# Kernel tuning notes

Measured on AMD Instinct MI355X. Metric: run time of the kernel, lower is better.

Reference implementation:

```python
import jax, jax.numpy as jnp
import numpy as np


def conv1x1(x, w, b):
    # x: [B, Cin, D, H, W], w: [Cout, Cin], b: [Cout]
    return jnp.einsum('bcdhw,oc->bodhw', x, w) + b[None, :, None, None, None]


def setup_inputs() -> dict:
    key = jax.random.key(0)
    ks = jax.random.split(key, 9)
    B, C, D, H, W = 2, 64, 16, 16, 16
    Cc = 64          # context_dim
    C8 = C // 8      # inner attention dim
    s = 0.05
    return {
        'x': jax.random.normal(ks[0], (B, C, D, H, W), jnp.float32),
        'context': jax.random.normal(ks[1], (B, Cc, D, H, W), jnp.float32),
        'Wq': jax.random.normal(ks[2], (C8, C), jnp.float32) * s,
        'bq': jax.random.normal(ks[3], (C8,), jnp.float32) * s,
        'Wk': jax.random.normal(ks[4], (C8, Cc), jnp.float32) * s,
        'bk': jax.random.normal(ks[5], (C8,), jnp.float32) * s,
        'Wv': jax.random.normal(ks[6], (C, Cc), jnp.float32) * s,
        'bv': jax.random.normal(ks[7], (C,), jnp.float32) * s,
        'gamma': jax.random.normal(ks[8], (1,), jnp.float32) * s,
    }


def reference(x, context, Wq, bq, Wk, bk, Wv, bv, gamma):
    B, C, D, H, W = x.shape
    N = D * H * W
    q = conv1x1(x, Wq, bq).reshape(B, -1, N)        # [B, C/8, N]
    k = conv1x1(context, Wk, bk).reshape(B, -1, N)  # [B, C/8, N]
    v = conv1x1(context, Wv, bv).reshape(B, C, N)   # [B, C, N]
    # energy[b, n, m] = q[:, :, n] . k[:, :, m]  (no scaling, as in source)
    energy = jnp.einsum('bcn,bcm->bnm', q, k)       # [B, N, N]
    attn = jax.nn.softmax(energy, axis=-1)
    # out = v @ attn^T : out[b, c, n] = sum_m v[b, c, m] * attn[b, n, m]
    out = jnp.einsum('bcm,bnm->bcn', v, attn).reshape(B, C, D, H, W)
    return gamma[0] * out + x
```

## Files before the change

### kernel.cpp

```cpp
#include <hip/hip_runtime.h>

#define NTOK 4096

typedef __attribute__((ext_vector_type(8))) short short8;
typedef __attribute__((ext_vector_type(4))) float f32x4;
typedef __attribute__((ext_vector_type(4))) unsigned int uint4v;

__device__ __forceinline__ unsigned short f2bf(float f) {
    unsigned u = __float_as_uint(f);
    u += 0x7fffu + ((u >> 16) & 1u);
    return (unsigned short)(u >> 16);
}

__device__ __forceinline__ unsigned int pk2(float lo, float hi) {
    return __builtin_amdgcn_perm(__float_as_uint(hi), __float_as_uint(lo), 0x07060302u);
}

__global__ __launch_bounds__(256) void proj(
    const float* __restrict__ x, const float* __restrict__ ctx,
    const float* __restrict__ Wq, const float* __restrict__ bq,
    const float* __restrict__ Wk, const float* __restrict__ bk,
    const float* __restrict__ Wv, const float* __restrict__ bv,
    unsigned short* __restrict__ qbf32, unsigned short* __restrict__ kbf32,
    unsigned short* __restrict__ vtp)
{
    __shared__ float sW[16 * 64];
    __shared__ float sB[16];
    int tid  = threadIdx.x;
    int ogrp = blockIdx.z;
    int b    = blockIdx.y;
    int n0   = blockIdx.x * 64;

    if (ogrp == 0) {
        for (int i = tid; i < 1024; i += 256)
            sW[i] = (i < 512) ? Wq[i] : Wk[i - 512];
        if (tid < 16) sB[tid] = (tid < 8) ? bq[tid] : bk[tid - 8];
    } else {
        for (int i = tid; i < 1024; i += 256)
            sW[i] = Wv[(ogrp - 1) * 1024 + i];
        if (tid < 16) sB[tid] = bv[(ogrp - 1) * 16 + tid];
    }
    __syncthreads();

    int nn   = tid & 63;
    int osub = tid >> 6;
    const float* inp = (ogrp == 0 && osub < 2) ? x : ctx;
    const float* ip  = inp + (size_t)b * 64 * NTOK + n0 + nn;

    float a0 = sB[osub * 4 + 0], a1 = sB[osub * 4 + 1];
    float a2 = sB[osub * 4 + 2], a3 = sB[osub * 4 + 3];
#pragma unroll 16
    for (int c = 0; c < 64; ++c) {
        float val = ip[(size_t)c * NTOK];
        a0 += sW[(osub * 4 + 0) * 64 + c] * val;
        a1 += sW[(osub * 4 + 1) * 64 + c] * val;
        a2 += sW[(osub * 4 + 2) * 64 + c] * val;
        a3 += sW[(osub * 4 + 3) * 64 + c] * val;
    }
    float av[4] = {a0, a1, a2, a3};

    if (ogrp == 0) {
        bool isq = osub < 2;
        float sc = isq ? 1.4426950408889634f : 1.0f;
        unsigned short* dst = isq ? qbf32 : kbf32;
        int half = osub & 1;
        size_t base = ((size_t)b * NTOK + n0 + nn) * 32;
        ushort4 pk = {f2bf(av[0] * sc), f2bf(av[1] * sc), f2bf(av[2] * sc), f2bf(av[3] * sc)};
        *(ushort4*)&dst[base + half * 4] = pk;
        ushort4 z = {0, 0, 0, 0};
        if (half == 0) {
            *(ushort4*)&dst[base + 8]  = z;
            *(ushort4*)&dst[base + 12] = z;
            *(ushort4*)&dst[base + 16] = z;
        } else {
            *(ushort4*)&dst[base + 20] = z;
            *(ushort4*)&dst[base + 24] = z;
            *(ushort4*)&dst[base + 28] = z;
        }
    } else {
        int cbase = (ogrp - 1) * 16 + osub * 4;
        int m  = n0 + nn;
        int g  = m & ~31;
        int mm = m & 31;
        int p  = ((mm >> 2) & 3) * 8 + (mm >> 4) * 4 + (mm & 3);
#pragma unroll
        for (int j = 0; j < 4; ++j)
            vtp[((size_t)b * 64 + cbase + j) * NTOK + g + p] = f2bf(av[j]);
    }
}

__global__ __launch_bounds__(512, 4) void attn3(
    const unsigned short* __restrict__ qbf32, const unsigned short* __restrict__ kbf32,
    const unsigned short* __restrict__ vtp, const float* __restrict__ x,
    const float* __restrict__ gamma, float* __restrict__ out)
{
    __shared__ float sO[8][64][17];
    __shared__ float sL[8][16];

    int tid  = threadIdx.x;
    int w    = tid >> 6, lane = tid & 63;
    int n    = lane & 15, quad = lane >> 4;
    int b    = blockIdx.y;
    int n0   = blockIdx.x * 16;

    const f32x4 z4 = {0.f, 0.f, 0.f, 0.f};
    short8 bq = *(const short8*)&qbf32[((size_t)b * NTOK + n0 + n) * 32 + quad * 8];

    const unsigned short* kb = kbf32 + (size_t)b * NTOK * 32;
    const unsigned short* vb = vtp   + (size_t)b * 64 * NTOK;
    int mbase = w * 512;

#define KLD(h, t) (*(const short8*)&kb[((size_t)(mbase + (h) * 64 + (t) * 16 + n)) * 32 + quad * 8])
#define VLD(h, s, ct) (*(const short8*)&vb[(size_t)((ct) * 16 + n) * NTOK + mbase + (h) * 64 + (s) * 32 + quad * 8])

    f32x4 acc0 = z4, acc1 = z4, acc2 = z4, acc3 = z4;
    float lsum = 0.f;

    short8 kf0 = KLD(0, 0), kf1 = KLD(0, 1), kf2 = KLD(0, 2), kf3 = KLD(0, 3);
    short8 af0 = VLD(0, 0, 0), af1 = VLD(0, 0, 1), af2 = VLD(0, 0, 2), af3 = VLD(0, 0, 3);
    short8 af4 = VLD(0, 1, 0), af5 = VLD(0, 1, 1), af6 = VLD(0, 1, 2), af7 = VLD(0, 1, 3);

    for (int h = 0; h < 8; ++h) {
        f32x4 sa0 = __builtin_amdgcn_mfma_f32_16x16x32_bf16(kf0, bq, z4, 0, 0, 0);
        f32x4 sa1 = __builtin_amdgcn_mfma_f32_16x16x32_bf16(kf1, bq, z4, 0, 0, 0);
        f32x4 sa2 = __builtin_amdgcn_mfma_f32_16x16x32_bf16(kf2, bq, z4, 0, 0, 0);
        f32x4 sa3 = __builtin_amdgcn_mfma_f32_16x16x32_bf16(kf3, bq, z4, 0, 0, 0);
        if (h < 7) {
            kf0 = KLD(h + 1, 0); kf1 = KLD(h + 1, 1);
            kf2 = KLD(h + 1, 2); kf3 = KLD(h + 1, 3);
        }

        float e00 = exp2f(sa0[0]), e01 = exp2f(sa0[1]), e02 = exp2f(sa0[2]), e03 = exp2f(sa0[3]);
        float e10 = exp2f(sa1[0]), e11 = exp2f(sa1[1]), e12 = exp2f(sa1[2]), e13 = exp2f(sa1[3]);
        float e20 = exp2f(sa2[0]), e21 = exp2f(sa2[1]), e22 = exp2f(sa2[2]), e23 = exp2f(sa2[3]);
        float e30 = exp2f(sa3[0]), e31 = exp2f(sa3[1]), e32 = exp2f(sa3[2]), e33 = exp2f(sa3[3]);
        lsum += ((e00 + e01) + (e02 + e03)) + ((e10 + e11) + (e12 + e13))
              + ((e20 + e21) + (e22 + e23)) + ((e30 + e31) + (e32 + e33));

        uint4v t0, t1;
        t0[0] = pk2(e00, e01); t0[1] = pk2(e02, e03);
        t0[2] = pk2(e10, e11); t0[3] = pk2(e12, e13);
        t1[0] = pk2(e20, e21); t1[1] = pk2(e22, e23);
        t1[2] = pk2(e30, e31); t1[3] = pk2(e32, e33);
        short8 pf0 = __builtin_bit_cast(short8, t0);
        short8 pf1 = __builtin_bit_cast(short8, t1);

        acc0 = __builtin_amdgcn_mfma_f32_16x16x32_bf16(af0, pf0, acc0, 0, 0, 0);
        acc1 = __builtin_amdgcn_mfma_f32_16x16x32_bf16(af1, pf0, acc1, 0, 0, 0);
        acc2 = __builtin_amdgcn_mfma_f32_16x16x32_bf16(af2, pf0, acc2, 0, 0, 0);
        acc3 = __builtin_amdgcn_mfma_f32_16x16x32_bf16(af3, pf0, acc3, 0, 0, 0);
        acc0 = __builtin_amdgcn_mfma_f32_16x16x32_bf16(af4, pf1, acc0, 0, 0, 0);
        acc1 = __builtin_amdgcn_mfma_f32_16x16x32_bf16(af5, pf1, acc1, 0, 0, 0);
        acc2 = __builtin_amdgcn_mfma_f32_16x16x32_bf16(af6, pf1, acc2, 0, 0, 0);
        acc3 = __builtin_amdgcn_mfma_f32_16x16x32_bf16(af7, pf1, acc3, 0, 0, 0);

        if (h < 7) {
            af0 = VLD(h + 1, 0, 0); af1 = VLD(h + 1, 0, 1);
            af2 = VLD(h + 1, 0, 2); af3 = VLD(h + 1, 0, 3);
            af4 = VLD(h + 1, 1, 0); af5 = VLD(h + 1, 1, 1);
            af6 = VLD(h + 1, 1, 2); af7 = VLD(h + 1, 1, 3);
        }
    }
#undef KLD
#undef VLD

    lsum += __shfl_xor(lsum, 16);
    lsum += __shfl_xor(lsum, 32);
    if (lane < 16) sL[w][n] = lsum;
    f32x4 acc[4] = {acc0, acc1, acc2, acc3};
#pragma unroll
    for (int ct = 0; ct < 4; ++ct)
#pragma unroll
        for (int r = 0; r < 4; ++r)
            sO[w][ct * 16 + quad * 4 + r][n] = acc[ct][r];
    __syncthreads();

    int c  = tid >> 3;
    int ng = (tid & 7) * 2;
    float g = gamma[0];
    float L0 = 0.f, L1 = 0.f, v0 = 0.f, v1 = 0.f;
#pragma unroll
    for (int w2 = 0; w2 < 8; ++w2) {
        L0 += sL[w2][ng];     L1 += sL[w2][ng + 1];
        v0 += sO[w2][c][ng];  v1 += sO[w2][c][ng + 1];
    }
    size_t ob = ((size_t)b * 64 + c) * NTOK + n0 + ng;
    float2 xv = *(const float2*)&x[ob];
    float2 ov = {g * (v0 / L0) + xv.x, g * (v1 / L1) + xv.y};
    *(float2*)&out[ob] = ov;
}

extern "C" void kernel_launch(void* const* d_in, const int* in_sizes, int n_in,
                              void* d_out, int out_size, void* d_ws, size_t ws_size,
                              hipStream_t stream) {
    const float* x     = (const float*)d_in[0];
    const float* ctx   = (const float*)d_in[1];
    const float* Wq    = (const float*)d_in[2];
    const float* bq    = (const float*)d_in[3];
    const float* Wk    = (const float*)d_in[4];
    const float* bk    = (const float*)d_in[5];
    const float* Wv    = (const float*)d_in[6];
    const float* bv    = (const float*)d_in[7];
    const float* gamma = (const float*)d_in[8];
    float* out = (float*)d_out;

    unsigned short* qbf32 = (unsigned short*)d_ws;
    unsigned short* kbf32 = qbf32 + 2 * NTOK * 32;
    unsigned short* vtp   = kbf32 + 2 * NTOK * 32;

    proj<<<dim3(64, 2, 5), 256, 0, stream>>>(x, ctx, Wq, bq, Wk, bk, Wv, bv, qbf32, kbf32, vtp);
    attn3<<<dim3(NTOK / 16, 2), 512, 0, stream>>>(qbf32, kbf32, vtp, x, gamma, out);
}
```

Before: 114.6 us.

## Compact Q/K to 8 bf16, split keys across 16 waves, use native exp2

Q and K are now stored as 8 bf16 values per token instead of a zero-padded 32. Only lanes with quad==0 load them, and the other lanes feed zeros into the MFMA, which cuts the memory traffic for padding and the zero-fill stores in the projection kernel. The attention kernel now runs 1024 threads with 16 waves, each covering 256 keys instead of 512, which doubles parallel work per block at the cost of more shared memory and a 16-way reduction. exp2f is replaced by the hardware exp2 builtin to avoid range-handling code.

```diff
diff --git a/kernel.cpp b/kernel.cpp
--- a/kernel.cpp
+++ b/kernel.cpp
@@ -21,7 +21,7 @@
     const float* __restrict__ Wq, const float* __restrict__ bq,
     const float* __restrict__ Wk, const float* __restrict__ bk,
     const float* __restrict__ Wv, const float* __restrict__ bv,
-    unsigned short* __restrict__ qbf32, unsigned short* __restrict__ kbf32,
+    unsigned short* __restrict__ qbf, unsigned short* __restrict__ kbf,
     unsigned short* __restrict__ vtp)
 {
     __shared__ float sW[16 * 64];
@@ -62,21 +62,10 @@
     if (ogrp == 0) {
         bool isq = osub < 2;
         float sc = isq ? 1.4426950408889634f : 1.0f;
-        unsigned short* dst = isq ? qbf32 : kbf32;
+        unsigned short* dst = isq ? qbf : kbf;
         int half = osub & 1;
-        size_t base = ((size_t)b * NTOK + n0 + nn) * 32;
         ushort4 pk = {f2bf(av[0] * sc), f2bf(av[1] * sc), f2bf(av[2] * sc), f2bf(av[3] * sc)};
-        *(ushort4*)&dst[base + half * 4] = pk;
-        ushort4 z = {0, 0, 0, 0};
-        if (half == 0) {
-            *(ushort4*)&dst[base + 8]  = z;
-            *(ushort4*)&dst[base + 12] = z;
-            *(ushort4*)&dst[base + 16] = z;
-        } else {
-            *(ushort4*)&dst[base + 20] = z;
-            *(ushort4*)&dst[base + 24] = z;
-            *(ushort4*)&dst[base + 28] = z;
-        }
+        *(ushort4*)&dst[((size_t)b * NTOK + n0 + nn) * 8 + half * 4] = pk;
     } else {
         int cbase = (ogrp - 1) * 16 + osub * 4;
         int m  = n0 + nn;
@@ -89,13 +78,13 @@
     }
 }
 
-__global__ __launch_bounds__(512, 4) void attn3(
-    const unsigned short* __restrict__ qbf32, const unsigned short* __restrict__ kbf32,
+__global__ __launch_bounds__(1024, 8) void attn4(
+    const unsigned short* __restrict__ qbf, const unsigned short* __restrict__ kbf,
     const unsigned short* __restrict__ vtp, const float* __restrict__ x,
     const float* __restrict__ gamma, float* __restrict__ out)
 {
-    __shared__ float sO[8][64][17];
-    __shared__ float sL[8][16];
+    __shared__ float sO[16][64][17];
+    __shared__ float sL[16][16];
 
     int tid  = threadIdx.x;
     int w    = tid >> 6, lane = tid & 63;
@@ -104,13 +93,17 @@
     int n0   = blockIdx.x * 16;
 
     const f32x4 z4 = {0.f, 0.f, 0.f, 0.f};
-    short8 bq = *(const short8*)&qbf32[((size_t)b * NTOK + n0 + n) * 32 + quad * 8];
-
-    const unsigned short* kb = kbf32 + (size_t)b * NTOK * 32;
-    const unsigned short* vb = vtp   + (size_t)b * 64 * NTOK;
-    int mbase = w * 512;
-
-#define KLD(h, t) (*(const short8*)&kb[((size_t)(mbase + (h) * 64 + (t) * 16 + n)) * 32 + quad * 8])
+    const short8 z8 = {0, 0, 0, 0, 0, 0, 0, 0};
+
+    short8 bq = z8;
+    if (quad == 0)
+        bq = *(const short8*)&qbf[((size_t)b * NTOK + n0 + n) * 8];
+
+    const unsigned short* kb = kbf + (size_t)b * NTOK * 8;
+    const unsigned short* vb = vtp + (size_t)b * 64 * NTOK;
+    int mbase = w * 256;
+
+#define KLD(h, t) (quad == 0 ? *(const short8*)&kb[(size_t)(mbase + (h) * 64 + (t) * 16 + n) * 8] : z8)
 #define VLD(h, s, ct) (*(const short8*)&vb[(size_t)((ct) * 16 + n) * NTOK + mbase + (h) * 64 + (s) * 32 + quad * 8])
 
     f32x4 acc0 = z4, acc1 = z4, acc2 = z4, acc3 = z4;
@@ -120,20 +113,24 @@
     short8 af0 = VLD(0, 0, 0), af1 = VLD(0, 0, 1), af2 = VLD(0, 0, 2), af3 = VLD(0, 0, 3);
     short8 af4 = VLD(0, 1, 0), af5 = VLD(0, 1, 1), af6 = VLD(0, 1, 2), af7 = VLD(0, 1, 3);
 
-    for (int h = 0; h < 8; ++h) {
+    for (int h = 0; h < 4; ++h) {
         f32x4 sa0 = __builtin_amdgcn_mfma_f32_16x16x32_bf16(kf0, bq, z4, 0, 0, 0);
         f32x4 sa1 = __builtin_amdgcn_mfma_f32_16x16x32_bf16(kf1, bq, z4, 0, 0, 0);
         f32x4 sa2 = __builtin_amdgcn_mfma_f32_16x16x32_bf16(kf2, bq, z4, 0, 0, 0);
         f32x4 sa3 = __builtin_amdgcn_mfma_f32_16x16x32_bf16(kf3, bq, z4, 0, 0, 0);
-        if (h < 7) {
+        if (h < 3) {
             kf0 = KLD(h + 1, 0); kf1 = KLD(h + 1, 1);
             kf2 = KLD(h + 1, 2); kf3 = KLD(h + 1, 3);
         }
 
-        float e00 = exp2f(sa0[0]), e01 = exp2f(sa0[1]), e02 = exp2f(sa0[2]), e03 = exp2f(sa0[3]);
-        float e10 = exp2f(sa1[0]), e11 = exp2f(sa1[1]), e12 = exp2f(sa1[2]), e13 = exp2f(sa1[3]);
-        float e20 = exp2f(sa2[0]), e21 = exp2f(sa2[1]), e22 = exp2f(sa2[2]), e23 = exp2f(sa2[3]);
-        float e30 = exp2f(sa3[0]), e31 = exp2f(sa3[1]), e32 = exp2f(sa3[2]), e33 = exp2f(sa3[3]);
+        float e00 = __builtin_amdgcn_exp2f(sa0[0]), e01 = __builtin_amdgcn_exp2f(sa0[1]);
+        float e02 = __builtin_amdgcn_exp2f(sa0[2]), e03 = __builtin_amdgcn_exp2f(sa0[3]);
+        float e10 = __builtin_amdgcn_exp2f(sa1[0]), e11 = __builtin_amdgcn_exp2f(sa1[1]);
+        float e12 = __builtin_amdgcn_exp2f(sa1[2]), e13 = __builtin_amdgcn_exp2f(sa1[3]);
+        float e20 = __builtin_amdgcn_exp2f(sa2[0]), e21 = __builtin_amdgcn_exp2f(sa2[1]);
+        float e22 = __builtin_amdgcn_exp2f(sa2[2]), e23 = __builtin_amdgcn_exp2f(sa2[3]);
+        float e30 = __builtin_amdgcn_exp2f(sa3[0]), e31 = __builtin_amdgcn_exp2f(sa3[1]);
+        float e32 = __builtin_amdgcn_exp2f(sa3[2]), e33 = __builtin_amdgcn_exp2f(sa3[3]);
         lsum += ((e00 + e01) + (e02 + e03)) + ((e10 + e11) + (e12 + e13))
               + ((e20 + e21) + (e22 + e23)) + ((e30 + e31) + (e32 + e33));
 
@@ -154,7 +151,7 @@
         acc2 = __builtin_amdgcn_mfma_f32_16x16x32_bf16(af6, pf1, acc2, 0, 0, 0);
         acc3 = __builtin_amdgcn_mfma_f32_16x16x32_bf16(af7, pf1, acc3, 0, 0, 0);
 
-        if (h < 7) {
+        if (h < 3) {
             af0 = VLD(h + 1, 0, 0); af1 = VLD(h + 1, 0, 1);
             af2 = VLD(h + 1, 0, 2); af3 = VLD(h + 1, 0, 3);
             af4 = VLD(h + 1, 1, 0); af5 = VLD(h + 1, 1, 1);
@@ -175,19 +172,17 @@
             sO[w][ct * 16 + quad * 4 + r][n] = acc[ct][r];
     __syncthreads();
 
-    int c  = tid >> 3;
-    int ng = (tid & 7) * 2;
+    int c  = tid >> 4;
+    int nn = tid & 15;
     float g = gamma[0];
-    float L0 = 0.f, L1 = 0.f, v0 = 0.f, v1 = 0.f;
-#pragma unroll
-    for (int w2 = 0; w2 < 8; ++w2) {
-        L0 += sL[w2][ng];     L1 += sL[w2][ng + 1];
-        v0 += sO[w2][c][ng];  v1 += sO[w2][c][ng + 1];
-    }
-    size_t ob = ((size_t)b * 64 + c) * NTOK + n0 + ng;
-    float2 xv = *(const float2*)&x[ob];
-    float2 ov = {g * (v0 / L0) + xv.x, g * (v1 / L1) + xv.y};
-    *(float2*)&out[ob] = ov;
+    float L = 0.f, val = 0.f;
+#pragma unroll
+    for (int w2 = 0; w2 < 16; ++w2) {
+        L   += sL[w2][nn];
+        val += sO[w2][c][nn];
+    }
+    size_t ob = ((size_t)b * 64 + c) * NTOK + n0 + nn;
+    out[ob] = g * (val / L) + x[ob];
 }
 
 extern "C" void kernel_launch(void* const* d_in, const int* in_sizes, int n_in,
@@ -204,10 +199,10 @@
     const float* gamma = (const float*)d_in[8];
     float* out = (float*)d_out;
 
-    unsigned short* qbf32 = (unsigned short*)d_ws;
-    unsigned short* kbf32 = qbf32 + 2 * NTOK * 32;
-    unsigned short* vtp   = kbf32 + 2 * NTOK * 32;
-
-    proj<<<dim3(64, 2, 5), 256, 0, stream>>>(x, ctx, Wq, bq, Wk, bk, Wv, bv, qbf32, kbf32, vtp);
-    attn3<<<dim3(NTOK / 16, 2), 512, 0, stream>>>(qbf32, kbf32, vtp, x, gamma, out);
-}
+    unsigned short* qbf = (unsigned short*)d_ws;
+    unsigned short* kbf = qbf + 2 * NTOK * 8;
+    unsigned short* vtp = kbf + 2 * NTOK * 8;
+
+    proj<<<dim3(64, 2, 5), 256, 0, stream>>>(x, ctx, Wq, bq, Wk, bk, Wv, bv, qbf, kbf, vtp);
+    attn4<<<dim3(NTOK / 16, 2), 1024, 0, stream>>>(qbf, kbf, vtp, x, gamma, out);
+}
```

After: 191.6 us. 1.67x slower.
